# Performance work log

Measured on AMD Instinct MI355X. Metric: run time of the kernel, lower is better.

The kernel has to match this reference:

```python
import jax, jax.numpy as jnp
import numpy as np

LOG2 = float(np.log(2.0))

def ssp(x):
    # shifted softplus: ln(0.5*exp(x) + 0.5) = softplus(x) - ln(2)
    return jax.nn.softplus(x) - LOG2

N, A, F, R, E = 50000, 128, 128, 20, 1600000

def setup_inputs() -> dict:
    key = jax.random.key(0)
    ks = jax.random.split(key, 14)
    s = lambda fan_in: 1.0 / np.sqrt(fan_in)
    return {
        "x": jax.random.normal(ks[0], (N, A), dtype=jnp.float32),
        "f_ij": jax.random.uniform(ks[1], (E, R), dtype=jnp.float32),
        "rcut_ij": jax.random.uniform(ks[2], (E,), dtype=jnp.float32),
        "idx_i": jnp.sort(jax.random.randint(ks[3], (E,), 0, N)),
        "idx_j": jax.random.randint(ks[4], (E,), 0, N),
        # in2f: Dense(A -> F), no bias
        "W_in2f": jax.random.uniform(ks[5], (A, F), minval=-s(A), maxval=s(A), dtype=jnp.float32),
        # filter_network: Dense(R->F, ssp) then Dense(F->F)
        "W_f1": jax.random.uniform(ks[6], (R, F), minval=-s(R), maxval=s(R), dtype=jnp.float32),
        "b_f1": jnp.zeros((F,), dtype=jnp.float32),
        "W_f2": jax.random.uniform(ks[7], (F, F), minval=-s(F), maxval=s(F), dtype=jnp.float32),
        "b_f2": jnp.zeros((F,), dtype=jnp.float32),
        # f2out: Dense(F->A, ssp) then Dense(A->A)
        "W_o1": jax.random.uniform(ks[8], (F, A), minval=-s(F), maxval=s(F), dtype=jnp.float32),
        "b_o1": jnp.zeros((A,), dtype=jnp.float32),
        "W_o2": jax.random.uniform(ks[9], (A, A), minval=-s(A), maxval=s(A), dtype=jnp.float32),
        "b_o2": jnp.zeros((A,), dtype=jnp.float32),
    }

def reference(x, f_ij, rcut_ij, idx_i, idx_j,
              W_in2f, W_f1, b_f1, W_f2, b_f2, W_o1, b_o1, W_o2, b_o2):
    n_atoms = x.shape[0]
    # in2f projection (no bias): [N, A] -> [N, F]
    h = x @ W_in2f
    # filter MLP on edge RBF features: [E, R] -> [E, F]
    Wij = ssp(f_ij @ W_f1 + b_f1) @ W_f2 + b_f2
    Wij = Wij * rcut_ij[:, None]
    # gather neighbor features, modulate by filter, scatter-add to centers
    x_ij = h[idx_j] * Wij                                   # [E, F]
    agg = jax.ops.segment_sum(x_ij, idx_i, num_segments=n_atoms)  # [N, F]
    # f2out MLP: [N, F] -> [N, A]
    out = ssp(agg @ W_o1 + b_o1) @ W_o2 + b_o2
    return out
```

## Files before the change

kernel.cpp:

```cpp
#include <hip/hip_runtime.h>
#include <math.h>

#define LN2F 0.6931471805599453f
#define LOG2EF 1.4426950408889634f

typedef _Float16 half_t;
typedef _Float16 half4_t __attribute__((ext_vector_type(4)));
typedef _Float16 half8_t __attribute__((ext_vector_type(8)));
typedef __fp16 fp16x2 __attribute__((ext_vector_type(2)));
typedef __fp16 fp16x4 __attribute__((ext_vector_type(4)));
typedef __fp16 fp16x8 __attribute__((ext_vector_type(8)));
typedef float f32x4 __attribute__((ext_vector_type(4)));

__device__ __forceinline__ float sspf(float z) {
    return fmaxf(z, 0.f) + __logf(1.f + __expf(-fabsf(z))) - LN2F;
}
__device__ __forceinline__ half4_t cvt4(float x, float y, float z, float w) {
    half4_t r; r[0]=(half_t)x; r[1]=(half_t)y; r[2]=(half_t)z; r[3]=(half_t)w; return r;
}
__device__ __forceinline__ half8_t pk8(float a, float b, float c, float d,
                                       float e, float f, float g, float h) {
    fp16x2 p0 = __builtin_amdgcn_cvt_pkrtz(a, b);
    fp16x2 p1 = __builtin_amdgcn_cvt_pkrtz(c, d);
    fp16x2 p2 = __builtin_amdgcn_cvt_pkrtz(e, f);
    fp16x2 p3 = __builtin_amdgcn_cvt_pkrtz(g, h);
    fp16x4 lo = __builtin_shufflevector(p0, p1, 0, 1, 2, 3);
    fp16x4 hi = __builtin_shufflevector(p2, p3, 0, 1, 2, 3);
    fp16x8 v  = __builtin_shufflevector(lo, hi, 0, 1, 2, 3, 4, 5, 6, 7);
    return __builtin_bit_cast(half8_t, v);
}

__device__ __forceinline__ void load_lds16(const void* g, void* l) {
    __builtin_amdgcn_global_load_lds(
        (const __attribute__((address_space(1))) unsigned int*)g,
        (__attribute__((address_space(3))) unsigned int*)l, 16, 0, 0);
}

__device__ __forceinline__ int lbound(const int* __restrict__ a, int n, int key) {
    int lo = 0, hi = n;
    while (lo < hi) { int m = (lo + hi) >> 1; if (a[m] < key) lo = m + 1; else hi = m; }
    return lo;
}

__global__ __launch_bounds__(256) void prep_weights(
    const float* __restrict__ W_in2f, const float* __restrict__ W_f1,
    const float* __restrict__ W_f2, const float* __restrict__ W_o1,
    const float* __restrict__ W_o2,
    const float* __restrict__ b_f1, const float* __restrict__ b_f2,
    half_t* __restrict__ Wt_in2f, half_t* __restrict__ Wt_f1,
    half_t* __restrict__ W2L, half_t* __restrict__ Wt_o1,
    half_t* __restrict__ Wt_o2, float* __restrict__ b1sc, float* __restrict__ b2a)
{
    int b = blockIdx.x;
    if (b < 64) {
        int i = b*256 + threadIdx.x;
        Wt_in2f[i] = (half_t)W_in2f[(i & 127)*128 + (i >> 7)];
    } else if (b < 80) {
        int i = (b-64)*256 + threadIdx.x;
        int n = i >> 5, k = i & 31;
        Wt_f1[i] = (k < 20) ? (half_t)W_f1[k*128 + n] : (half_t)0.f;
    } else if (b < 144) {
        int i = (b-80)*256 + threadIdx.x;
        int j = i & 7, ln = (i >> 3) & 15, g = (i >> 7) & 3;
        int nt = (i >> 9) & 7, t = i >> 12;
        int k = 32*t + ((j < 4) ? (g*4 + j) : (16 + g*4 + (j - 4)));
        W2L[i] = (half_t)(LN2F * W_f2[k*128 + ln*8 + nt]);
    } else if (b < 208) {
        int i = (b-144)*256 + threadIdx.x;
        Wt_o1[i] = (half_t)W_o1[(i & 127)*128 + (i >> 7)];
    } else if (b < 272) {
        int i = (b-208)*256 + threadIdx.x;
        Wt_o2[i] = (half_t)W_o2[(i & 127)*128 + (i >> 7)];
    } else {
        int c = threadIdx.x;
        if (c < 128) {
            float s = 0.f;
            for (int k = 0; k < 128; ++k) s += W_f2[k*128 + c];
            b2a[c]  = b_f2[c] - LN2F * s;
            b1sc[c] = b_f1[c] * LOG2EF;
        }
    }
}

__global__ __launch_bounds__(256) void seg_starts(
    const int* __restrict__ idx_i, int* __restrict__ atom_start, int E, int N)
{
    int e = blockIdx.x * 256 + threadIdx.x;
    if (e >= E) return;
    int a = idx_i[e];
    int prev = (e == 0) ? -1 : idx_i[e - 1];
    for (int k = prev + 1; k <= a; ++k) atom_start[k] = e;
    if (e == E - 1)
        for (int k = a + 1; k <= N; ++k) atom_start[k] = E;
}

__global__ __launch_bounds__(256) void mfma_gemm_h(
    const float* __restrict__ A, const half_t* __restrict__ Bt,
    half_t* __restrict__ Ch, int nrows)
{
    const int tid = threadIdx.x;
    const int w = tid >> 6, l = tid & 63, g = l >> 4, ln = l & 15;
    const int r0 = blockIdx.x * 64;

    f32x4 acc[4][2];
    #pragma unroll
    for (int rf = 0; rf < 4; ++rf)
        #pragma unroll
        for (int cf = 0; cf < 2; ++cf) acc[rf][cf] = (f32x4)0.f;

    #pragma unroll
    for (int kk = 0; kk < 8; ++kk) {
        const int kb = kk * 16 + g * 4;
        half4_t a[4];
        #pragma unroll
        for (int rf = 0; rf < 4; ++rf) {
            int r = r0 + rf * 16 + ln;
            int rr = r < nrows ? r : nrows - 1;
            float4 av = *(const float4*)(A + (size_t)rr * 128 + kb);
            a[rf] = cvt4(av.x, av.y, av.z, av.w);
        }
        #pragma unroll
        for (int cf = 0; cf < 2; ++cf) {
            int n = w * 32 + cf * 16 + ln;
            half4_t b = *(const half4_t*)(Bt + (size_t)n * 128 + kb);
            #pragma unroll
            for (int rf = 0; rf < 4; ++rf)
                acc[rf][cf] = __builtin_amdgcn_mfma_f32_16x16x16f16(a[rf], b, acc[rf][cf], 0, 0, 0);
        }
    }
    #pragma unroll
    for (int cf = 0; cf < 2; ++cf) {
        int n = w * 32 + cf * 16 + ln;
        #pragma unroll
        for (int rf = 0; rf < 4; ++rf)
            #pragma unroll
            for (int reg = 0; reg < 4; ++reg) {
                int r = r0 + rf * 16 + g * 4 + reg;
                if (r < nrows) Ch[(size_t)r * 128 + n] = (half_t)acc[rf][cf][reg];
            }
    }
}

__global__ __launch_bounds__(256) void mfma_gemm2(
    const float* __restrict__ A, const half_t* __restrict__ Bt1,
    const float* __restrict__ bias1, const half_t* __restrict__ Bt2,
    const float* __restrict__ bias2, float* __restrict__ out, int nrows)
{
    __shared__ half_t ts[64][136];
    const int tid = threadIdx.x;
    const int w = tid >> 6, l = tid & 63, g = l >> 4, ln = l & 15;
    const int r0 = blockIdx.x * 64;

    f32x4 acc[4][2];
    #pragma unroll
    for (int rf = 0; rf < 4; ++rf)
        #pragma unroll
        for (int cf = 0; cf < 2; ++cf) acc[rf][cf] = (f32x4)0.f;
    #pragma unroll
    for (int kk = 0; kk < 8; ++kk) {
        const int kb = kk * 16 + g * 4;
        half4_t a[4];
        #pragma unroll
        for (int rf = 0; rf < 4; ++rf) {
            int r = r0 + rf * 16 + ln;
            int rr = r < nrows ? r : nrows - 1;
            float4 av = *(const float4*)(A + (size_t)rr * 128 + kb);
            a[rf] = cvt4(av.x, av.y, av.z, av.w);
        }
        #pragma unroll
        for (int cf = 0; cf < 2; ++cf) {
            int n = w * 32 + cf * 16 + ln;
            half4_t b = *(const half4_t*)(Bt1 + (size_t)n * 128 + kb);
            #pragma unroll
            for (int rf = 0; rf < 4; ++rf)
                acc[rf][cf] = __builtin_amdgcn_mfma_f32_16x16x16f16(a[rf], b, acc[rf][cf], 0, 0, 0);
        }
    }
    #pragma unroll
    for (int cf = 0; cf < 2; ++cf) {
        int n = w * 32 + cf * 16 + ln;
        float bv = bias1[n];
        #pragma unroll
        for (int rf = 0; rf < 4; ++rf)
            #pragma unroll
            for (int reg = 0; reg < 4; ++reg)
                ts[rf*16 + g*4 + reg][n] = (half_t)sspf(acc[rf][cf][reg] + bv);
    }
    __syncthreads();

    f32x4 acc2[4][2];
    #pragma unroll
    for (int rf = 0; rf < 4; ++rf)
        #pragma unroll
        for (int cf = 0; cf < 2; ++cf) acc2[rf][cf] = (f32x4)0.f;
    #pragma unroll
    for (int kk = 0; kk < 8; ++kk) {
        const int kb = kk * 16 + g * 4;
        half4_t a[4];
        #pragma unroll
        for (int rf = 0; rf < 4; ++rf)
            a[rf] = *(const half4_t*)&ts[rf*16 + ln][kb];
        #pragma unroll
        for (int cf = 0; cf < 2; ++cf) {
            int n = w * 32 + cf * 16 + ln;
            half4_t b = *(const half4_t*)(Bt2 + (size_t)n * 128 + kb);
            #pragma unroll
            for (int rf = 0; rf < 4; ++rf)
                acc2[rf][cf] = __builtin_amdgcn_mfma_f32_16x16x16f16(a[rf], b, acc2[rf][cf], 0, 0, 0);
        }
    }
    #pragma unroll
    for (int cf = 0; cf < 2; ++cf) {
        int n = w * 32 + cf * 16 + ln;
        float bv = bias2[n];
        #pragma unroll
        for (int rf = 0; rf < 4; ++rf)
            #pragma unroll
            for (int reg = 0; reg < 4; ++reg) {
                int r = r0 + rf * 16 + g * 4 + reg;
                if (r < nrows) out[(size_t)r * 128 + n] = acc2[rf][cf][reg] + bv;
            }
    }
}

__global__ __launch_bounds__(256, 3) void edge_kernel(
    const float* __restrict__ f_ij, const float* __restrict__ rcut,
    const int* __restrict__ idx_j,
    const half_t* __restrict__ Wt_f1, const float* __restrict__ b1sc,
    const half_t* __restrict__ W2L, const float* __restrict__ b2a,
    const half_t* __restrict__ hh, float* __restrict__ agg,
    const int* __restrict__ atom_start, int E, int N, int W)
{
    __shared__ __align__(16) half_t W2s[16384];
    __shared__ __align__(16) half_t hsh[4][2048];
    __shared__ float b1s[128];

    const int tid = threadIdx.x;
    const int w = tid >> 6, l = tid & 63, g = l >> 4, ln = l & 15;

    for (int i = tid; i < 2048; i += 256)
        ((float4*)W2s)[i] = ((const float4*)W2L)[i];
    if (tid < 128) b1s[tid] = b1sc[tid];
    __syncthreads();

    const int kg = blockIdx.x * 4 + w;
    const int aLo = lbound(atom_start, N + 1, (int)((size_t)kg * E / W));
    const int aHi = (kg == W - 1) ? N
                  : lbound(atom_start, N + 1, (int)((size_t)(kg + 1) * E / W));
    if (aLo >= aHi) return;

    half8_t w1f[8];
    #pragma unroll
    for (int rf = 0; rf < 8; ++rf) {
        half4_t lo = *(const half4_t*)(Wt_f1 + (size_t)(rf*16 + ln)*32 + g*4);
        half4_t hi = *(const half4_t*)(Wt_f1 + (size_t)(rf*16 + ln)*32 + 16 + g*4);
        w1f[rf] = __builtin_shufflevector(lo, hi, 0, 1, 2, 3, 4, 5, 6, 7);
    }

    f32x4 b2acc[8];
    {
        float4 blo4 = *(const float4*)(b2a + ln*8);
        float4 bhi4 = *(const float4*)(b2a + ln*8 + 4);
        float bv[8] = {blo4.x, blo4.y, blo4.z, blo4.w, bhi4.x, bhi4.y, bhi4.z, bhi4.w};
        #pragma unroll
        for (int q = 0; q < 8; ++q) {
            f32x4 t = {bv[q], bv[q], bv[q], bv[q]};
            b2acc[q] = t;
        }
    }

    int acur = aLo;
    int ends0 = atom_start[acur + 1];
    int ends1 = atom_start[min(acur + 2, N)];
    int ends2 = atom_start[min(acur + 3, N)];
    int cs = atom_start[acur];

    int jv[4]; float4 fA, fB; float rc[4];
    #pragma unroll
    for (int it = 0; it < 4; ++it)
        jv[it] = idx_j[min(cs + 4*it + g, E - 1)];
    {
        int e = min(cs + ln, E - 1);
        fA = *(const float4*)(f_ij + (size_t)e*20 + g*4);
        fB = *(const float4*)(f_ij + (size_t)e*20 + 16);
    }
    #pragma unroll
    for (int r2 = 0; r2 < 4; ++r2) rc[r2] = rcut[min(cs + 4*g + r2, E - 1)];
    asm volatile("" ::: "memory");

    float racc[8];
    #pragma unroll
    for (int q = 0; q < 8; ++q) racc[q] = 0.f;

    while (acur < aHi) {
        const int ce = min(cs + 16, ends0);
        const int csn = ce;
        const bool flushF = (ce == ends0);

        asm volatile("" ::: "memory");
        #pragma unroll
        for (int it = 0; it < 4; ++it)
            load_lds16(hh + (size_t)jv[it]*128 + ((ln ^ it) << 3),
                       &hsh[w][it*512]);
        asm volatile("" ::: "memory");

        half4_t blo = cvt4(fA.x, fA.y, fA.z, fA.w);
        half4_t bhi;
        if (g == 0) bhi = cvt4(fB.x, fB.y, fB.z, fB.w);
        else { half4_t zz = {}; bhi = zz; }
        half8_t bf = __builtin_shufflevector(blo, bhi, 0, 1, 2, 3, 4, 5, 6, 7);
        float rcm[4];
        #pragma unroll
        for (int r2 = 0; r2 < 4; ++r2)
            rcm[r2] = (cs + 4*g + r2 < ce) ? rc[r2] : 0.f;

        int jvn[4];
        #pragma unroll
        for (int it = 0; it < 4; ++it)
            jvn[it] = idx_j[min(csn + 4*it + g, E - 1)];
        float4 fA1, fB1;
        {
            int e = min(csn + ln, E - 1);
            fA1 = *(const float4*)(f_ij + (size_t)e*20 + g*4);
            fB1 = *(const float4*)(f_ij + (size_t)e*20 + 16);
        }
        float rc1[4];
        #pragma unroll
        for (int r2 = 0; r2 < 4; ++r2) rc1[r2] = rcut[min(csn + 4*g + r2, E - 1)];
        const int aeL = atom_start[min(acur + 4, N)];
        asm volatile("" ::: "memory");

        f32x4 z[8];
        #pragma unroll
        for (int rf = 0; rf < 8; ++rf)
            z[rf] = __builtin_amdgcn_mfma_f32_16x16x32_f16(w1f[rf], bf, (f32x4)0.f, 0, 0, 0);
        half8_t a2[4];
        #pragma unroll
        for (int t = 0; t < 4; ++t) {
            float4 bbA = *(const float4*)&b1s[(2*t)*16 + g*4];
            float4 bbB = *(const float4*)&b1s[(2*t+1)*16 + g*4];
            float l0 = __log2f(1.f + exp2f(fmaf(z[2*t][0],   LOG2EF, bbA.x)));
            float l1 = __log2f(1.f + exp2f(fmaf(z[2*t][1],   LOG2EF, bbA.y)));
            float l2 = __log2f(1.f + exp2f(fmaf(z[2*t][2],   LOG2EF, bbA.z)));
            float l3 = __log2f(1.f + exp2f(fmaf(z[2*t][3],   LOG2EF, bbA.w)));
            float l4 = __log2f(1.f + exp2f(fmaf(z[2*t+1][0], LOG2EF, bbB.x)));
            float l5 = __log2f(1.f + exp2f(fmaf(z[2*t+1][1], LOG2EF, bbB.y)));
            float l6 = __log2f(1.f + exp2f(fmaf(z[2*t+1][2], LOG2EF, bbB.z)));
            float l7 = __log2f(1.f + exp2f(fmaf(z[2*t+1][3], LOG2EF, bbB.w)));
            a2[t] = pk8(l0, l1, l2, l3, l4, l5, l6, l7);
        }

        f32x4 acc[8];
        #pragma unroll
        for (int q = 0; q < 8; ++q) acc[q] = b2acc[q];
        __builtin_amdgcn_s_setprio(1);
        #pragma unroll
        for (int t = 0; t < 4; ++t)
            #pragma unroll
            for (int q = 0; q < 8; ++q) {
                half8_t bw = *(const half8_t*)&W2s[(((t*8 + q)*4 + g)*16 + ln)*8];
                acc[q] = __builtin_amdgcn_mfma_f32_16x16x32_f16(a2[t], bw, acc[q], 0, 0, 0);
            }
        __builtin_amdgcn_s_setprio(0);

        asm volatile("s_waitcnt vmcnt(4)" ::: "memory");
        __builtin_amdgcn_sched_barrier(0);

        #pragma unroll
        for (int r2 = 0; r2 < 4; ++r2) {
            half8_t hv8 = *(const half8_t*)&hsh[w][(4*g + r2)*128 + ((ln ^ g) << 3)];
            float rr = rcm[r2];
            #pragma unroll
            for (int q = 0; q < 8; ++q)
                racc[q] = fmaf(acc[q][r2] * rr, (float)hv8[q], racc[q]);
        }

        if (flushF) {
            #pragma unroll
            for (int q = 0; q < 8; ++q) {
                float r = racc[q];
                r += __shfl_xor(r, 16, 64);
                r += __shfl_xor(r, 32, 64);
                racc[q] = r;
            }
            if (g == 0) {
                float4 v0 = {racc[0], racc[1], racc[2], racc[3]};
                float4 v1 = {racc[4], racc[5], racc[6], racc[7]};
                *(float4*)(agg + (size_t)acur*128 + ln*8)     = v0;
                *(float4*)(agg + (size_t)acur*128 + ln*8 + 4) = v1;
            }
            #pragma unroll
            for (int q = 0; q < 8; ++q) racc[q] = 0.f;
            ++acur;
            ends0 = ends1; ends1 = ends2; ends2 = aeL;
        }

        cs = csn;
        #pragma unroll
        for (int it = 0; it < 4; ++it) jv[it] = jvn[it];
        fA = fA1; fB = fB1;
        #pragma unroll
        for (int r2 = 0; r2 < 4; ++r2) rc[r2] = rc1[r2];
    }
}

extern "C" void kernel_launch(void* const* d_in, const int* in_sizes, int n_in,
                              void* d_out, int out_size, void* d_ws, size_t ws_size,
                              hipStream_t stream)
{
    const float* x      = (const float*)d_in[0];
    const float* f_ij   = (const float*)d_in[1];
    const float* rcut   = (const float*)d_in[2];
    const int*   idx_i  = (const int*)d_in[3];
    const int*   idx_j  = (const int*)d_in[4];
    const float* W_in2f = (const float*)d_in[5];
    const float* W_f1   = (const float*)d_in[6];
    const float* b_f1   = (const float*)d_in[7];
    const float* W_f2   = (const float*)d_in[8];
    const float* b_f2   = (const float*)d_in[9];
    const float* W_o1   = (const float*)d_in[10];
    const float* b_o1   = (const float*)d_in[11];
    const float* W_o2   = (const float*)d_in[12];
    const float* b_o2   = (const float*)d_in[13];

    const int N = in_sizes[0] / 128;
    const int E = in_sizes[2];

    half_t* h16  = (half_t*)d_ws;
    half_t* wt   = (half_t*)((char*)d_ws + (size_t)N * 128 * 4);
    half_t* Wt_in2f = wt;
    half_t* Wt_f1   = wt + 16384;
    half_t* W2L     = wt + 16384 + 4096;
    half_t* Wt_o1   = W2L + 16384;
    half_t* Wt_o2   = Wt_o1 + 16384;
    float*  b1sc    = (float*)(Wt_o2 + 16384);
    float*  b2a     = b1sc + 128;
    int* atom_start = (int*)(b2a + 128);

    prep_weights<<<273, 256, 0, stream>>>(W_in2f, W_f1, W_f2, W_o1, W_o2,
                                          b_f1, b_f2,
                                          Wt_in2f, Wt_f1, W2L, Wt_o1, Wt_o2,
                                          b1sc, b2a);
    seg_starts<<<(E + 255) / 256, 256, 0, stream>>>(idx_i, atom_start, E, N);

    const int gn  = (N + 63) / 64;
    const int nbl = 768;
    const int W   = nbl * 4;

    mfma_gemm_h<<<gn, 256, 0, stream>>>(x, Wt_in2f, h16, N);

    edge_kernel<<<nbl, 256, 0, stream>>>(f_ij, rcut, idx_j,
                                         Wt_f1, b1sc, W2L, b2a,
                                         h16, (float*)d_out, atom_start, E, N, W);

    mfma_gemm2<<<gn, 256, 0, stream>>>((const float*)d_out, Wt_o1, b_o1,
                                       Wt_o2, b_o2, (float*)d_out, N);
}
```

Baseline: 282.3 us.

## Precompute per-atom edge chunk metadata and double-buffer neighbor gathers in edge kernel

Adds preprocessing kernels that split each atom's edges into 16-edge chunks. They build chunk offsets with a scan, per-chunk metadata (start, count, atom, flush flag) and pre-shifted neighbor byte offsets, so the edge kernel loops over chunks instead of tracking atom boundaries. The LDS gather buffer for h is now double-buffered so the next chunk's neighbor rows load while the current chunk computes. Work is balanced by chunk count rather than edge count, and the grid drops to 512 blocks at occupancy 2. This costs three extra small launches, one of them a single-block serial scan, plus extra workspace traffic, and lower occupancy may reduce latency hiding.

```diff
diff --git a/kernel.cpp b/kernel.cpp
--- a/kernel.cpp
+++ b/kernel.cpp
@@ -94,6 +94,70 @@
         for (int k = a + 1; k <= N; ++k) atom_start[k] = E;
 }
 
+__global__ __launch_bounds__(256) void chunk_scan(
+    const int* __restrict__ atom_start, int* __restrict__ chunk_off, int N)
+{
+    __shared__ int part[256];
+    __shared__ int base[257];
+    int t = threadIdx.x;
+    int L = (N + 255) / 256;
+    int lo = min(t * L, N), hi = min(lo + L, N);
+    int s = 0;
+    for (int a = lo; a < hi; ++a) {
+        int deg = atom_start[a+1] - atom_start[a];
+        s += max(1, (deg + 15) >> 4);
+    }
+    part[t] = s;
+    __syncthreads();
+    if (t == 0) {
+        int acc = 0;
+        for (int i = 0; i < 256; ++i) { base[i] = acc; acc += part[i]; }
+        base[256] = acc;
+    }
+    __syncthreads();
+    int run = base[t];
+    for (int a = lo; a < hi; ++a) {
+        chunk_off[a] = run;
+        int deg = atom_start[a+1] - atom_start[a];
+        run += max(1, (deg + 15) >> 4);
+    }
+    if (t == 0) chunk_off[N] = base[256];
+}
+
+__global__ __launch_bounds__(256) void chunk_atoms(
+    const int* __restrict__ atom_start, const int* __restrict__ chunk_off,
+    int2* __restrict__ cmeta, int N)
+{
+    int a = blockIdx.x * 256 + threadIdx.x;
+    if (a >= N) return;
+    int s = atom_start[a], e1 = atom_start[a+1];
+    int c0 = chunk_off[a], nc = chunk_off[a+1] - c0;
+    for (int k = 0; k < nc; ++k) {
+        int cs = s + 16*k;
+        int cnt = e1 - cs; cnt = cnt < 0 ? 0 : (cnt > 16 ? 16 : cnt);
+        cmeta[c0+k] = make_int2(cs, (a << 6) | (cnt << 1) | (k == nc-1 ? 1 : 0));
+    }
+}
+
+__global__ __launch_bounds__(256) void chunk_edges(
+    const int* __restrict__ idx_j, const int* __restrict__ chunk_off,
+    int2* __restrict__ cmeta, int* __restrict__ jvpk, int N, int ncmax)
+{
+    int i = blockIdx.x * 256 + threadIdx.x;
+    if (i >= ncmax * 16) return;
+    int c = i >> 4, s = i & 15;
+    int NC = chunk_off[N];
+    if (c >= NC) {
+        jvpk[i] = 0;
+        if (s == 0) cmeta[c] = make_int2(0, 0);
+        return;
+    }
+    int2 m = cmeta[c];
+    int cnt = (m.y >> 1) & 31;
+    int off = 4*(s & 3) + (s >> 2);
+    jvpk[i] = (off < cnt) ? (idx_j[m.x + off] << 8) : 0;
+}
+
 __global__ __launch_bounds__(256) void mfma_gemm_h(
     const float* __restrict__ A, const half_t* __restrict__ Bt,
     half_t* __restrict__ Ch, int nrows)
@@ -223,16 +287,16 @@
     }
 }
 
-__global__ __launch_bounds__(256, 3) void edge_kernel(
+__global__ __launch_bounds__(256, 2) void edge_kernel(
     const float* __restrict__ f_ij, const float* __restrict__ rcut,
-    const int* __restrict__ idx_j,
+    const int2* __restrict__ cmeta, const int* __restrict__ jvpk,
     const half_t* __restrict__ Wt_f1, const float* __restrict__ b1sc,
     const half_t* __restrict__ W2L, const float* __restrict__ b2a,
     const half_t* __restrict__ hh, float* __restrict__ agg,
-    const int* __restrict__ atom_start, int E, int N, int W)
+    const int* __restrict__ chunk_off, int E, int N, int W)
 {
     __shared__ __align__(16) half_t W2s[16384];
-    __shared__ __align__(16) half_t hsh[4][2048];
+    __shared__ __align__(16) half_t hsh[4][2][2048];
     __shared__ float b1s[128];
 
     const int tid = threadIdx.x;
@@ -243,11 +307,14 @@
     if (tid < 128) b1s[tid] = b1sc[tid];
     __syncthreads();
 
+    const int NC = chunk_off[N];
     const int kg = blockIdx.x * 4 + w;
-    const int aLo = lbound(atom_start, N + 1, (int)((size_t)kg * E / W));
+    const int aLo = lbound(chunk_off, N + 1, (int)((size_t)kg * NC / W));
     const int aHi = (kg == W - 1) ? N
-                  : lbound(atom_start, N + 1, (int)((size_t)(kg + 1) * E / W));
-    if (aLo >= aHi) return;
+                  : lbound(chunk_off, N + 1, (int)((size_t)(kg + 1) * NC / W));
+    int c  = __builtin_amdgcn_readfirstlane(chunk_off[aLo]);
+    const int c1 = __builtin_amdgcn_readfirstlane(chunk_off[aHi]);
+    if (c >= c1) return;
 
     half8_t w1f[8];
     #pragma unroll
@@ -269,65 +336,74 @@
         }
     }
 
-    int acur = aLo;
-    int ends0 = atom_start[acur + 1];
-    int ends1 = atom_start[min(acur + 2, N)];
-    int ends2 = atom_start[min(acur + 3, N)];
-    int cs = atom_start[acur];
-
-    int jv[4]; float4 fA, fB; float rc[4];
-    #pragma unroll
-    for (int it = 0; it < 4; ++it)
-        jv[it] = idx_j[min(cs + 4*it + g, E - 1)];
+    const char* hb = (const char*)hh;
+    const int sw0 = (ln ^ 0) << 4, sw1 = (ln ^ 1) << 4;
+    const int sw2 = (ln ^ 2) << 4, sw3 = (ln ^ 3) << 4;
+
+    int4 jvC = *(const int4*)(jvpk + (size_t)c*16 + g*4);
+    int2 mC  = cmeta[c];
+    asm volatile("" ::: "memory");
+    load_lds16(hb + (unsigned)jvC.x + sw0, &hsh[w][0][0]);
+    load_lds16(hb + (unsigned)jvC.y + sw1, &hsh[w][0][512]);
+    load_lds16(hb + (unsigned)jvC.z + sw2, &hsh[w][0][1024]);
+    load_lds16(hb + (unsigned)jvC.w + sw3, &hsh[w][0][1536]);
+    asm volatile("" ::: "memory");
+    float4 fA, fB; float rc[4];
     {
-        int e = min(cs + ln, E - 1);
+        int cs0 = __builtin_amdgcn_readfirstlane(mC.x);
+        int e = min(cs0 + ln, E - 1);
         fA = *(const float4*)(f_ij + (size_t)e*20 + g*4);
         fB = *(const float4*)(f_ij + (size_t)e*20 + 16);
-    }
-    #pragma unroll
-    for (int r2 = 0; r2 < 4; ++r2) rc[r2] = rcut[min(cs + 4*g + r2, E - 1)];
+        #pragma unroll
+        for (int r2 = 0; r2 < 4; ++r2)
+            rc[r2] = rcut[min(cs0 + 4*g + r2, E - 1)];
+    }
+    int m1cur = mC.y;
+    int4 jvN = *(const int4*)(jvpk + (size_t)(c+1)*16 + g*4);
+    int2 mN  = cmeta[c+1];
     asm volatile("" ::: "memory");
 
     float racc[8];
     #pragma unroll
     for (int q = 0; q < 8; ++q) racc[q] = 0.f;
-
-    while (acur < aHi) {
-        const int ce = min(cs + 16, ends0);
-        const int csn = ce;
-        const bool flushF = (ce == ends0);
-
+    int p = 0;
+
+    while (c < c1) {
         asm volatile("" ::: "memory");
-        #pragma unroll
-        for (int it = 0; it < 4; ++it)
-            load_lds16(hh + (size_t)jv[it]*128 + ((ln ^ it) << 3),
-                       &hsh[w][it*512]);
-        asm volatile("" ::: "memory");
+        {
+            half_t* d = &hsh[w][p^1][0];
+            load_lds16(hb + (unsigned)jvN.x + sw0, d);
+            load_lds16(hb + (unsigned)jvN.y + sw1, d + 512);
+            load_lds16(hb + (unsigned)jvN.z + sw2, d + 1024);
+            load_lds16(hb + (unsigned)jvN.w + sw3, d + 1536);
+        }
+        asm volatile("s_waitcnt vmcnt(4)" ::: "memory");
+        __builtin_amdgcn_sched_barrier(0);
 
         half4_t blo = cvt4(fA.x, fA.y, fA.z, fA.w);
         half4_t bhi;
         if (g == 0) bhi = cvt4(fB.x, fB.y, fB.z, fB.w);
         else { half4_t zz = {}; bhi = zz; }
         half8_t bf = __builtin_shufflevector(blo, bhi, 0, 1, 2, 3, 4, 5, 6, 7);
+        const int mw  = __builtin_amdgcn_readfirstlane(m1cur);
+        const int cnt = (mw >> 1) & 31;
         float rcm[4];
         #pragma unroll
         for (int r2 = 0; r2 < 4; ++r2)
-            rcm[r2] = (cs + 4*g + r2 < ce) ? rc[r2] : 0.f;
-
-        int jvn[4];
-        #pragma unroll
-        for (int it = 0; it < 4; ++it)
-            jvn[it] = idx_j[min(csn + 4*it + g, E - 1)];
-        float4 fA1, fB1;
+            rcm[r2] = (4*g + r2 < cnt) ? rc[r2] : 0.f;
+
+        int4 jv2 = *(const int4*)(jvpk + (size_t)(c+2)*16 + g*4);
+        int2 m2  = cmeta[c+2];
+        float4 fA1, fB1; float rc1[4];
         {
+            int csn = __builtin_amdgcn_readfirstlane(mN.x);
             int e = min(csn + ln, E - 1);
             fA1 = *(const float4*)(f_ij + (size_t)e*20 + g*4);
             fB1 = *(const float4*)(f_ij + (size_t)e*20 + 16);
-        }
-        float rc1[4];
-        #pragma unroll
-        for (int r2 = 0; r2 < 4; ++r2) rc1[r2] = rcut[min(csn + 4*g + r2, E - 1)];
-        const int aeL = atom_start[min(acur + 4, N)];
+            #pragma unroll
+            for (int r2 = 0; r2 < 4; ++r2)
+                rc1[r2] = rcut[min(csn + 4*g + r2, E - 1)];
+        }
         asm volatile("" ::: "memory");
 
         f32x4 z[8];
@@ -363,19 +439,24 @@
             }
         __builtin_amdgcn_s_setprio(0);
 
-        asm volatile("s_waitcnt vmcnt(4)" ::: "memory");
-        __builtin_amdgcn_sched_barrier(0);
-
-        #pragma unroll
-        for (int r2 = 0; r2 < 4; ++r2) {
-            half8_t hv8 = *(const half8_t*)&hsh[w][(4*g + r2)*128 + ((ln ^ g) << 3)];
-            float rr = rcm[r2];
-            #pragma unroll
-            for (int q = 0; q < 8; ++q)
-                racc[q] = fmaf(acc[q][r2] * rr, (float)hv8[q], racc[q]);
-        }
-
-        if (flushF) {
+        {
+            const half_t* hb0 = &hsh[w][p][(4*g)*128 + ((ln ^ g) << 3)];
+            half8_t h0 = *(const half8_t*)(hb0);
+            half8_t h1 = *(const half8_t*)(hb0 + 128);
+            half8_t h2 = *(const half8_t*)(hb0 + 256);
+            half8_t h3 = *(const half8_t*)(hb0 + 384);
+            #pragma unroll
+            for (int q = 0; q < 8; ++q) {
+                float s = racc[q];
+                s = fmaf(acc[q][0] * rcm[0], (float)h0[q], s);
+                s = fmaf(acc[q][1] * rcm[1], (float)h1[q], s);
+                s = fmaf(acc[q][2] * rcm[2], (float)h2[q], s);
+                s = fmaf(acc[q][3] * rcm[3], (float)h3[q], s);
+                racc[q] = s;
+            }
+        }
+
+        if (mw & 1) {
             #pragma unroll
             for (int q = 0; q < 8; ++q) {
                 float r = racc[q];
@@ -383,24 +464,22 @@
                 r += __shfl_xor(r, 32, 64);
                 racc[q] = r;
             }
+            int arow = mw >> 6;
             if (g == 0) {
                 float4 v0 = {racc[0], racc[1], racc[2], racc[3]};
                 float4 v1 = {racc[4], racc[5], racc[6], racc[7]};
-                *(float4*)(agg + (size_t)acur*128 + ln*8)     = v0;
-                *(float4*)(agg + (size_t)acur*128 + ln*8 + 4) = v1;
+                *(float4*)(agg + (size_t)arow*128 + ln*8)     = v0;
+                *(float4*)(agg + (size_t)arow*128 + ln*8 + 4) = v1;
             }
             #pragma unroll
             for (int q = 0; q < 8; ++q) racc[q] = 0.f;
-            ++acur;
-            ends0 = ends1; ends1 = ends2; ends2 = aeL;
-        }
-
-        cs = csn;
-        #pragma unroll
-        for (int it = 0; it < 4; ++it) jv[it] = jvn[it];
-        fA = fA1; fB = fB1;
+        }
+
+        jvN = jv2; fA = fA1; fB = fB1;
         #pragma unroll
         for (int r2 = 0; r2 < 4; ++r2) rc[r2] = rc1[r2];
+        m1cur = mN.y; mN = m2;
+        p ^= 1; ++c;
     }
 }
 
@@ -425,9 +504,10 @@
 
     const int N = in_sizes[0] / 128;
     const int E = in_sizes[2];
+    const int NCMAX = E/16 + N + 8;
 
     half_t* h16  = (half_t*)d_ws;
-    half_t* wt   = (half_t*)((char*)d_ws + (size_t)N * 128 * 4);
+    half_t* wt   = (half_t*)((char*)d_ws + (size_t)N * 128 * 2);
     half_t* Wt_in2f = wt;
     half_t* Wt_f1   = wt + 16384;
     half_t* W2L     = wt + 16384 + 4096;
@@ -436,22 +516,31 @@
     float*  b1sc    = (float*)(Wt_o2 + 16384);
     float*  b2a     = b1sc + 128;
     int* atom_start = (int*)(b2a + 128);
+    int* chunk_off  = atom_start + (N + 1);
+    int* ip = chunk_off + (N + 1);
+    if (((uintptr_t)ip) & 7) ++ip;
+    int2*  cmeta = (int2*)ip;
+    int*   jvpk  = (int*)(cmeta + NCMAX);
 
     prep_weights<<<273, 256, 0, stream>>>(W_in2f, W_f1, W_f2, W_o1, W_o2,
                                           b_f1, b_f2,
                                           Wt_in2f, Wt_f1, W2L, Wt_o1, Wt_o2,
                                           b1sc, b2a);
     seg_starts<<<(E + 255) / 256, 256, 0, stream>>>(idx_i, atom_start, E, N);
+    chunk_scan<<<1, 256, 0, stream>>>(atom_start, chunk_off, N);
+    chunk_atoms<<<(N + 255) / 256, 256, 0, stream>>>(atom_start, chunk_off, cmeta, N);
+    chunk_edges<<<(NCMAX * 16 + 255) / 256, 256, 0, stream>>>(
+        idx_j, chunk_off, cmeta, jvpk, N, NCMAX);
 
     const int gn  = (N + 63) / 64;
-    const int nbl = 768;
+    const int nbl = 512;
     const int W   = nbl * 4;
 
     mfma_gemm_h<<<gn, 256, 0, stream>>>(x, Wt_in2f, h16, N);
 
-    edge_kernel<<<nbl, 256, 0, stream>>>(f_ij, rcut, idx_j,
+    edge_kernel<<<nbl, 256, 0, stream>>>(f_ij, rcut, cmeta, jvpk,
                                          Wt_f1, b1sc, W2L, b2a,
-                                         h16, (float*)d_out, atom_start, E, N, W);
+                                         h16, (float*)d_out, chunk_off, E, N, W);
 
     mfma_gemm2<<<gn, 256, 0, stream>>>((const float*)d_out, Wt_o1, b_o1,
                                        Wt_o2, b_o2, (float*)d_out, N);
```

Result: slower. 350.9 us (+24.3%).
